# Kernel optimization log

Measured on AMD Instinct MI355X. Metric: run time of the kernel, lower is better.

The kernel has to match this reference:

```python
import jax, jax.numpy as jnp
import numpy as np

H = 10          # hidden_dim
OUT = 100       # linear output (charset logits)
STEPS = 30      # decoder steps
START = 1.0     # Alphabet.start_integer
NL = 3          # num_layers
B, L, TD, AD = 8192, 32, 63, 1
IN = TD + AD


def setup_inputs() -> dict:
    key = jax.random.key(0)
    ks = iter(jax.random.split(key, 64))
    s = 0.3
    d = {}
    d["families"] = jnp.zeros((B,), jnp.int32)
    d["languages"] = jnp.zeros((B,), jnp.int32)
    d["tags"] = jax.random.uniform(next(ks), (B, TD), jnp.float32)
    d["lemmata"] = jax.random.uniform(next(ks), (B, L), jnp.float32)
    for pre in ("enc", "dec"):
        for l in range(NL):
            din = IN if l == 0 else H
            d[f"{pre}_W_ih{l}"] = jax.random.normal(next(ks), (4 * H, din), jnp.float32) * s
            d[f"{pre}_W_hh{l}"] = jax.random.normal(next(ks), (4 * H, H), jnp.float32) * s
            d[f"{pre}_b_ih{l}"] = jax.random.normal(next(ks), (4 * H,), jnp.float32) * s
            d[f"{pre}_b_hh{l}"] = jax.random.normal(next(ks), (4 * H,), jnp.float32) * s
    d["lin_W"] = jax.random.normal(next(ks), (OUT, H), jnp.float32) * s
    d["lin_b"] = jnp.zeros((OUT,), jnp.float32)
    return d


def _lstm_cell(layers, h, c, x):
    # torch LSTM gate order: i, f, g, o. Dropout inactive in eval mode.
    nh, nc, inp = [], [], x
    for (W_ih, W_hh, b_ih, b_hh), hl, cl in zip(layers, h, c):
        g = inp @ W_ih.T + hl @ W_hh.T + b_ih + b_hh  # (B, 4H)
        i_, f_, g_, o_ = jnp.split(g, 4, axis=-1)
        cl = jax.nn.sigmoid(f_) * cl + jax.nn.sigmoid(i_) * jnp.tanh(g_)
        hl = jax.nn.sigmoid(o_) * jnp.tanh(cl)
        nh.append(hl); nc.append(cl); inp = hl
    return tuple(nh), tuple(nc), inp


def _forward(tags, lemmata, enc, dec, lin_W, lin_b):
    Bb, Ll = lemmata.shape
    # time-major encoder input: feature order [char, tags...] -> (L, B, 1+TD)
    xs = jnp.concatenate([lemmata.T[:, :, None],
                          jnp.broadcast_to(tags[None], (Ll, Bb, tags.shape[1]))], axis=-1)
    h = tuple(jnp.zeros((Bb, H), lemmata.dtype) for _ in range(NL))
    c = h

    def estep(carry, x):
        hh, cc = carry
        hh, cc, _ = _lstm_cell(enc, hh, cc, x)
        return (hh, cc), None

    (h, c), _ = jax.lax.scan(estep, (h, c), xs)

    tok = jnp.full((Bb,), START, lemmata.dtype)

    def dstep(carry, _):
        hh, cc, t = carry
        x = jnp.concatenate([t[:, None], tags], axis=-1)  # (B, 1+TD)
        hh, cc, y = _lstm_cell(dec, hh, cc, x)
        probs = jax.nn.sigmoid(y @ lin_W.T + lin_b)       # (B, 100)
        nt = jax.lax.stop_gradient(jnp.argmax(probs, axis=-1))
        return (hh, cc, nt.astype(t.dtype)), (probs, nt)

    _, (probs, toks) = jax.lax.scan(dstep, (h, c, tok), None, length=STEPS)
    return jnp.transpose(probs, (1, 0, 2)), toks.T  # (B,30,100), (B,30)


def reference(families, languages, tags, lemmata,
              enc_W_ih0, enc_W_hh0, enc_b_ih0, enc_b_hh0,
              enc_W_ih1, enc_W_hh1, enc_b_ih1, enc_b_hh1,
              enc_W_ih2, enc_W_hh2, enc_b_ih2, enc_b_hh2,
              dec_W_ih0, dec_W_hh0, dec_b_ih0, dec_b_hh0,
              dec_W_ih1, dec_W_hh1, dec_b_ih1, dec_b_hh1,
              dec_W_ih2, dec_W_hh2, dec_b_ih2, dec_b_hh2,
              lin_W, lin_b):
    enc = ((enc_W_ih0, enc_W_hh0, enc_b_ih0, enc_b_hh0),
           (enc_W_ih1, enc_W_hh1, enc_b_ih1, enc_b_hh1),
           (enc_W_ih2, enc_W_hh2, enc_b_ih2, enc_b_hh2))
    dec = ((dec_W_ih0, dec_W_hh0, dec_b_ih0, dec_b_hh0),
           (dec_W_ih1, dec_W_hh1, dec_b_ih1, dec_b_hh1),
           (dec_W_ih2, dec_W_hh2, dec_b_ih2, dec_b_hh2))
    return _forward(tags, lemmata, enc, dec, lin_W, lin_b)
```

## Files before the change

### kernel.cpp

```cpp
#include <hip/hip_runtime.h>
#include <cmath>

#define DEV __device__ __forceinline__

static DEV float fast_exp2(float x) {
#if __has_builtin(__builtin_amdgcn_exp2f)
  return __builtin_amdgcn_exp2f(x);
#else
  return exp2f(x);
#endif
}
static DEV float fast_rcp(float x) {
#if __has_builtin(__builtin_amdgcn_rcpf)
  return __builtin_amdgcn_rcpf(x);
#else
  return 1.0f / x;
#endif
}

#define LOG2E 1.4426950408889634f

static DEV float rdl(float x, int l) {
  return __int_as_float(__builtin_amdgcn_readlane(__float_as_int(x), l));
}

template <int K>
static DEV float qb(float x) {
  return __int_as_float(
      __builtin_amdgcn_update_dpp(0, __float_as_int(x), K * 0x55, 0xF, 0xF, true));
}

struct KP {
  const float* tags; const float* lem;
  const float* eWih0; const float* eWhh0; const float* ebih0; const float* ebhh0;
  const float* eWih1; const float* eWhh1; const float* ebih1; const float* ebhh1;
  const float* eWih2; const float* eWhh2; const float* ebih2; const float* ebhh2;
  const float* dWih0; const float* dWhh0; const float* dbih0; const float* dbhh0;
  const float* dWih1; const float* dWhh1; const float* dbih1; const float* dbhh1;
  const float* dWih2; const float* dWhh2; const float* dbih2; const float* dbhh2;
  const float* linW; const float* linb;
  float* outp; float* outt;
  int B;
};

__global__ __launch_bounds__(256) void seq2seq_kernel(KP P) {
  const int tid = threadIdx.x;
  const int lane = tid & 63;
  const int b = blockIdx.x * 4 + (tid >> 6);

  __shared__ float sW[5040];
  for (int i = tid; i < 5040; i += 256) {
    int m = (i >= 2520) ? 1 : 0;
    int r2 = i - m * 2520;
    int rr = r2 / 63;
    int dd = r2 - rr * 63;
    sW[i] = (m ? P.dWih0 : P.eWih0)[rr * 64 + 1 + dd];
  }
  __syncthreads();
  if (b >= P.B) return;

  const int jq = lane >> 2;
  const int kg = lane & 3;
  const int jj = (jq < 10) ? jq : 9;
  const int row = kg * 10 + jj;

  const float kc = (kg == 2) ? (-2.0f * LOG2E) : (-LOG2E);
  const float am = (kg == 2) ? 2.0f : 1.0f;
  const float ab = (kg == 2) ? -1.0f : 0.0f;

  auto act = [&](float g) -> float {
    float y = fast_rcp(1.0f + fast_exp2(g * kc));
    return fmaf(am, y, ab);
  };

  float tv = (lane < 63) ? P.tags[(size_t)b * 63 + lane] : 0.0f;
  float lemv = (lane < 32) ? P.lem[(size_t)b * 32 + lane] : 0.0f;

  float ew0c = P.eWih0[row * 64];
  float ehh0[10], eih1[10], ehh1[10], eih2[10], ehh2[10];
#pragma unroll
  for (int q = 0; q < 10; q++) {
    ehh0[q] = P.eWhh0[row * 10 + q];
    eih1[q] = P.eWih1[row * 10 + q];
    ehh1[q] = P.eWhh1[row * 10 + q];
    eih2[q] = P.eWih2[row * 10 + q];
    ehh2[q] = P.eWhh2[row * 10 + q];
  }
  float pre0 = P.ebih0[row] + P.ebhh0[row];
  float pre1 = P.ebih1[row] + P.ebhh1[row];
  float pre2 = P.ebih2[row] + P.ebhh2[row];
  float dpre0 = P.dbih0[row] + P.dbhh0[row];

  {
    const int ro = row * 63;
#pragma unroll
    for (int d = 0; d < 63; d++) {
      float ts = rdl(tv, d);
      pre0 = fmaf(sW[ro + d], ts, pre0);
      dpre0 = fmaf(sW[2520 + ro + d], ts, dpre0);
    }
  }

  float h0[10], h1[10], h2[10];
#pragma unroll
  for (int q = 0; q < 10; q++) { h0[q] = 0.0f; h1[q] = 0.0f; h2[q] = 0.0f; }
  float c0 = 0.0f, c1 = 0.0f, c2 = 0.0f;

  auto update = [&](float a, float& c, float (&h)[10]) {
    float a0 = qb<0>(a);
    float a1 = qb<1>(a);
    float a2 = qb<2>(a);
    float a3 = qb<3>(a);
    c = a1 * c + a0 * a2;
    float y = fast_rcp(1.0f + fast_exp2(c * (-2.0f * LOG2E)));
    float hv = a3 * fmaf(2.0f, y, -1.0f);
#pragma unroll
    for (int q = 0; q < 10; q++) h[q] = rdl(hv, 4 * q);
  };

  for (int t = 0; t < 32; t++) {
    float ch = rdl(lemv, t);
    float g = fmaf(ew0c, ch, pre0);
#pragma unroll
    for (int q = 0; q < 10; q++) g = fmaf(ehh0[q], h0[q], g);
    update(act(g), c0, h0);

    g = pre1;
#pragma unroll
    for (int q = 0; q < 10; q++) g = fmaf(eih1[q], h0[q], g);
#pragma unroll
    for (int q = 0; q < 10; q++) g = fmaf(ehh1[q], h1[q], g);
    update(act(g), c1, h1);

    g = pre2;
#pragma unroll
    for (int q = 0; q < 10; q++) g = fmaf(eih2[q], h1[q], g);
#pragma unroll
    for (int q = 0; q < 10; q++) g = fmaf(ehh2[q], h2[q], g);
    update(act(g), c2, h2);
  }

  float dw0c = P.dWih0[row * 64];
  float dhh0[10], dih1[10], dhh1[10], dih2[10], dhh2[10];
#pragma unroll
  for (int q = 0; q < 10; q++) {
    dhh0[q] = P.dWhh0[row * 10 + q];
    dih1[q] = P.dWih1[row * 10 + q];
    dhh1[q] = P.dWhh1[row * 10 + q];
    dih2[q] = P.dWih2[row * 10 + q];
    dhh2[q] = P.dWhh2[row * 10 + q];
  }
  float dpre1 = P.dbih1[row] + P.dbhh1[row];
  float dpre2 = P.dbih2[row] + P.dbhh2[row];

  const int lr1 = lane;
  const int lr2 = (lane < 36) ? (64 + lane) : 99;
  float lw0[10], lw1[10];
#pragma unroll
  for (int q = 0; q < 10; q++) {
    lw0[q] = P.linW[lr1 * 10 + q];
    lw1[q] = P.linW[lr2 * 10 + q];
  }
  float lb0 = P.linb[lr1];
  float lb1 = (lane < 36) ? P.linb[lr2] : -1e30f;

  float* op0 = P.outp + (size_t)b * 3000;
  float tok = 1.0f;
  float tokv = 0.0f;

  for (int s = 0; s < 30; s++) {
    float g = fmaf(dw0c, tok, dpre0);
#pragma unroll
    for (int q = 0; q < 10; q++) g = fmaf(dhh0[q], h0[q], g);
    update(act(g), c0, h0);

    g = dpre1;
#pragma unroll
    for (int q = 0; q < 10; q++) g = fmaf(dih1[q], h0[q], g);
#pragma unroll
    for (int q = 0; q < 10; q++) g = fmaf(dhh1[q], h1[q], g);
    update(act(g), c1, h1);

    g = dpre2;
#pragma unroll
    for (int q = 0; q < 10; q++) g = fmaf(dih2[q], h1[q], g);
#pragma unroll
    for (int q = 0; q < 10; q++) g = fmaf(dhh2[q], h2[q], g);
    update(act(g), c2, h2);

    float z0 = lb0, z1 = lb1;
#pragma unroll
    for (int q = 0; q < 10; q++) {
      z0 = fmaf(lw0[q], h2[q], z0);
      z1 = fmaf(lw1[q], h2[q], z1);
    }
    float p0 = fast_rcp(1.0f + fast_exp2(z0 * (-LOG2E)));
    float p1 = fast_rcp(1.0f + fast_exp2(z1 * (-LOG2E)));

    float* op = op0 + s * 100;
    op[lane] = p0;
    if (lane < 36) op[64 + lane] = p1;

    float vm = p0; int im = lane;
    if (p1 > vm) { vm = p1; im = 64 + lane; }
#pragma unroll
    for (int off = 32; off > 0; off >>= 1) {
      float vo = __shfl_xor(vm, off);
      int io = __shfl_xor(im, off);
      if (vo > vm || (vo == vm && io < im)) { vm = vo; im = io; }
    }
    im = __builtin_amdgcn_readfirstlane(im);
    tok = (float)im;
    tokv = (lane == s) ? tok : tokv;
  }

  if (lane < 30) P.outt[(size_t)b * 30 + lane] = tokv;
}

extern "C" void kernel_launch(void* const* d_in, const int* in_sizes, int n_in,
                              void* d_out, int out_size, void* d_ws, size_t ws_size,
                              hipStream_t stream) {
  KP P;
  P.tags = (const float*)d_in[2];
  P.lem = (const float*)d_in[3];
  P.eWih0 = (const float*)d_in[4];  P.eWhh0 = (const float*)d_in[5];
  P.ebih0 = (const float*)d_in[6];  P.ebhh0 = (const float*)d_in[7];
  P.eWih1 = (const float*)d_in[8];  P.eWhh1 = (const float*)d_in[9];
  P.ebih1 = (const float*)d_in[10]; P.ebhh1 = (const float*)d_in[11];
  P.eWih2 = (const float*)d_in[12]; P.eWhh2 = (const float*)d_in[13];
  P.ebih2 = (const float*)d_in[14]; P.ebhh2 = (const float*)d_in[15];
  P.dWih0 = (const float*)d_in[16]; P.dWhh0 = (const float*)d_in[17];
  P.dbih0 = (const float*)d_in[18]; P.dbhh0 = (const float*)d_in[19];
  P.dWih1 = (const float*)d_in[20]; P.dWhh1 = (const float*)d_in[21];
  P.dbih1 = (const float*)d_in[22]; P.dbhh1 = (const float*)d_in[23];
  P.dWih2 = (const float*)d_in[24]; P.dWhh2 = (const float*)d_in[25];
  P.dbih2 = (const float*)d_in[26]; P.dbhh2 = (const float*)d_in[27];
  P.linW = (const float*)d_in[28];
  P.linb = (const float*)d_in[29];

  const int B = in_sizes[3] / 32;
  P.B = B;
  P.outp = (float*)d_out;
  P.outt = P.outp + (size_t)B * 3000;

  const int blocks = (B + 3) / 4;
  seq2seq_kernel<<<dim3(blocks), dim3(256), 0, stream>>>(P);
}
```

Before: 180.9 us.

## Drop LDS weight staging, split dot-product chains, and use DPP argmax

The shared-memory staging of the layer-0 tag weights and its block barrier are removed. The tag projection is now computed from float4 global loads with readlane broadcasts. Each gate dot product uses two accumulators to shorten the FMA dependency chain. The shuffle-based argmax becomes a DPP row-shift max reduction followed by ballots and a count-trailing-zeros to pick the first maximal index. The DPP max and ballot path should cut the latency of each decoder step, but global loads in place of LDS could add some memory latency, and the tie handling now relies on exact float equality.

```diff
diff --git a/kernel.cpp b/kernel.cpp
--- a/kernel.cpp
+++ b/kernel.cpp
@@ -28,6 +28,23 @@
 static DEV float qb(float x) {
   return __int_as_float(
       __builtin_amdgcn_update_dpp(0, __float_as_int(x), K * 0x55, 0xF, 0xF, true));
+}
+
+template <int CTRL>
+static DEV float dppmax(float x) {
+  float o = __int_as_float(
+      __builtin_amdgcn_update_dpp(0, __float_as_int(x), CTRL, 0xF, 0xF, true));
+  return fmaxf(x, o);
+}
+
+static DEV float wavemax_bcast(float m) {
+  m = dppmax<0x111>(m);
+  m = dppmax<0x112>(m);
+  m = dppmax<0x114>(m);
+  m = dppmax<0x118>(m);
+  m = dppmax<0x142>(m);
+  m = dppmax<0x143>(m);
+  return rdl(m, 63);
 }
 
 struct KP {
@@ -47,16 +64,6 @@
   const int tid = threadIdx.x;
   const int lane = tid & 63;
   const int b = blockIdx.x * 4 + (tid >> 6);
-
-  __shared__ float sW[5040];
-  for (int i = tid; i < 5040; i += 256) {
-    int m = (i >= 2520) ? 1 : 0;
-    int r2 = i - m * 2520;
-    int rr = r2 / 63;
-    int dd = r2 - rr * 63;
-    sW[i] = (m ? P.dWih0 : P.eWih0)[rr * 64 + 1 + dd];
-  }
-  __syncthreads();
   if (b >= P.B) return;
 
   const int jq = lane >> 2;
@@ -76,7 +83,29 @@
   float tv = (lane < 63) ? P.tags[(size_t)b * 63 + lane] : 0.0f;
   float lemv = (lane < 32) ? P.lem[(size_t)b * 32 + lane] : 0.0f;
 
-  float ew0c = P.eWih0[row * 64];
+  float pre0 = P.ebih0[row] + P.ebhh0[row];
+  float dpre0 = P.dbih0[row] + P.dbhh0[row];
+  float ew0c, dw0c;
+  {
+    const float4* e4 = (const float4*)P.eWih0 + row * 16;
+    const float4* d4 = (const float4*)P.dWih0 + row * 16;
+    float4 we = e4[0], wd = d4[0];
+    ew0c = we.x; dw0c = wd.x;
+    float t0 = rdl(tv, 0), t1 = rdl(tv, 1), t2 = rdl(tv, 2);
+    pre0 = fmaf(we.y, t0, pre0); pre0 = fmaf(we.z, t1, pre0); pre0 = fmaf(we.w, t2, pre0);
+    dpre0 = fmaf(wd.y, t0, dpre0); dpre0 = fmaf(wd.z, t1, dpre0); dpre0 = fmaf(wd.w, t2, dpre0);
+#pragma unroll
+    for (int c = 1; c < 16; c++) {
+      float4 e = e4[c], d = d4[c];
+      int dd = 4 * c - 1;
+      float u0 = rdl(tv, dd), u1 = rdl(tv, dd + 1), u2 = rdl(tv, dd + 2), u3 = rdl(tv, dd + 3);
+      pre0 = fmaf(e.x, u0, pre0); pre0 = fmaf(e.y, u1, pre0);
+      pre0 = fmaf(e.z, u2, pre0); pre0 = fmaf(e.w, u3, pre0);
+      dpre0 = fmaf(d.x, u0, dpre0); dpre0 = fmaf(d.y, u1, dpre0);
+      dpre0 = fmaf(d.z, u2, dpre0); dpre0 = fmaf(d.w, u3, dpre0);
+    }
+  }
+
   float ehh0[10], eih1[10], ehh1[10], eih2[10], ehh2[10];
 #pragma unroll
   for (int q = 0; q < 10; q++) {
@@ -86,20 +115,8 @@
     eih2[q] = P.eWih2[row * 10 + q];
     ehh2[q] = P.eWhh2[row * 10 + q];
   }
-  float pre0 = P.ebih0[row] + P.ebhh0[row];
   float pre1 = P.ebih1[row] + P.ebhh1[row];
   float pre2 = P.ebih2[row] + P.ebhh2[row];
-  float dpre0 = P.dbih0[row] + P.dbhh0[row];
-
-  {
-    const int ro = row * 63;
-#pragma unroll
-    for (int d = 0; d < 63; d++) {
-      float ts = rdl(tv, d);
-      pre0 = fmaf(sW[ro + d], ts, pre0);
-      dpre0 = fmaf(sW[2520 + ro + d], ts, dpre0);
-    }
-  }
 
   float h0[10], h1[10], h2[10];
 #pragma unroll
@@ -111,36 +128,48 @@
     float a1 = qb<1>(a);
     float a2 = qb<2>(a);
     float a3 = qb<3>(a);
-    c = a1 * c + a0 * a2;
+    c = fmaf(a1, c, a0 * a2);
     float y = fast_rcp(1.0f + fast_exp2(c * (-2.0f * LOG2E)));
     float hv = a3 * fmaf(2.0f, y, -1.0f);
 #pragma unroll
     for (int q = 0; q < 10; q++) h[q] = rdl(hv, 4 * q);
   };
 
+  auto dot2 = [&](const float (&wa)[10], const float (&ha)[10],
+                  const float (&wb)[10], const float (&hb)[10], float pre) -> float {
+    float ga = pre, gb = 0.0f;
+#pragma unroll
+    for (int q = 0; q < 10; q += 2) {
+      ga = fmaf(wa[q], ha[q], ga);
+      gb = fmaf(wa[q + 1], ha[q + 1], gb);
+    }
+#pragma unroll
+    for (int q = 0; q < 10; q += 2) {
+      ga = fmaf(wb[q], hb[q], ga);
+      gb = fmaf(wb[q + 1], hb[q + 1], gb);
+    }
+    return ga + gb;
+  };
+  auto dot1 = [&](const float (&w)[10], const float (&h)[10], float pre) -> float {
+    float ga = pre, gb = 0.0f;
+#pragma unroll
+    for (int q = 0; q < 10; q += 2) {
+      ga = fmaf(w[q], h[q], ga);
+      gb = fmaf(w[q + 1], h[q + 1], gb);
+    }
+    return ga + gb;
+  };
+
   for (int t = 0; t < 32; t++) {
     float ch = rdl(lemv, t);
-    float g = fmaf(ew0c, ch, pre0);
-#pragma unroll
-    for (int q = 0; q < 10; q++) g = fmaf(ehh0[q], h0[q], g);
+    float g = dot1(ehh0, h0, fmaf(ew0c, ch, pre0));
     update(act(g), c0, h0);
-
-    g = pre1;
-#pragma unroll
-    for (int q = 0; q < 10; q++) g = fmaf(eih1[q], h0[q], g);
-#pragma unroll
-    for (int q = 0; q < 10; q++) g = fmaf(ehh1[q], h1[q], g);
+    g = dot2(eih1, h0, ehh1, h1, pre1);
     update(act(g), c1, h1);
-
-    g = pre2;
-#pragma unroll
-    for (int q = 0; q < 10; q++) g = fmaf(eih2[q], h1[q], g);
-#pragma unroll
-    for (int q = 0; q < 10; q++) g = fmaf(ehh2[q], h2[q], g);
+    g = dot2(eih2, h1, ehh2, h2, pre2);
     update(act(g), c2, h2);
   }
 
-  float dw0c = P.dWih0[row * 64];
   float dhh0[10], dih1[10], dhh1[10], dih2[10], dhh2[10];
 #pragma unroll
   for (int q = 0; q < 10; q++) {
@@ -153,15 +182,14 @@
   float dpre1 = P.dbih1[row] + P.dbhh1[row];
   float dpre2 = P.dbih2[row] + P.dbhh2[row];
 
-  const int lr1 = lane;
   const int lr2 = (lane < 36) ? (64 + lane) : 99;
   float lw0[10], lw1[10];
 #pragma unroll
   for (int q = 0; q < 10; q++) {
-    lw0[q] = P.linW[lr1 * 10 + q];
+    lw0[q] = P.linW[lane * 10 + q];
     lw1[q] = P.linW[lr2 * 10 + q];
   }
-  float lb0 = P.linb[lr1];
+  float lb0 = P.linb[lane];
   float lb1 = (lane < 36) ? P.linb[lr2] : -1e30f;
 
   float* op0 = P.outp + (size_t)b * 3000;
@@ -169,31 +197,15 @@
   float tokv = 0.0f;
 
   for (int s = 0; s < 30; s++) {
-    float g = fmaf(dw0c, tok, dpre0);
-#pragma unroll
-    for (int q = 0; q < 10; q++) g = fmaf(dhh0[q], h0[q], g);
+    float g = dot1(dhh0, h0, fmaf(dw0c, tok, dpre0));
     update(act(g), c0, h0);
-
-    g = dpre1;
-#pragma unroll
-    for (int q = 0; q < 10; q++) g = fmaf(dih1[q], h0[q], g);
-#pragma unroll
-    for (int q = 0; q < 10; q++) g = fmaf(dhh1[q], h1[q], g);
+    g = dot2(dih1, h0, dhh1, h1, dpre1);
     update(act(g), c1, h1);
-
-    g = dpre2;
-#pragma unroll
-    for (int q = 0; q < 10; q++) g = fmaf(dih2[q], h1[q], g);
-#pragma unroll
-    for (int q = 0; q < 10; q++) g = fmaf(dhh2[q], h2[q], g);
+    g = dot2(dih2, h1, dhh2, h2, dpre2);
     update(act(g), c2, h2);
 
-    float z0 = lb0, z1 = lb1;
-#pragma unroll
-    for (int q = 0; q < 10; q++) {
-      z0 = fmaf(lw0[q], h2[q], z0);
-      z1 = fmaf(lw1[q], h2[q], z1);
-    }
+    float z0 = dot1(lw0, h2, lb0);
+    float z1 = dot1(lw1, h2, lb1);
     float p0 = fast_rcp(1.0f + fast_exp2(z0 * (-LOG2E)));
     float p1 = fast_rcp(1.0f + fast_exp2(z1 * (-LOG2E)));
 
@@ -201,15 +213,10 @@
     op[lane] = p0;
     if (lane < 36) op[64 + lane] = p1;
 
-    float vm = p0; int im = lane;
-    if (p1 > vm) { vm = p1; im = 64 + lane; }
-#pragma unroll
-    for (int off = 32; off > 0; off >>= 1) {
-      float vo = __shfl_xor(vm, off);
-      int io = __shfl_xor(im, off);
-      if (vo > vm || (vo == vm && io < im)) { vm = vo; im = io; }
-    }
-    im = __builtin_amdgcn_readfirstlane(im);
+    float vm = wavemax_bcast(fmaxf(p0, p1));
+    unsigned long long m0 = __ballot(p0 == vm);
+    unsigned long long m1 = __ballot(p1 == vm);
+    int im = m0 ? (int)__builtin_ctzll(m0) : 64 + (int)__builtin_ctzll(m1);
     tok = (float)im;
     tokv = (lane == s) ? tok : tokv;
   }
```

Result: faster. 175.0 us (-3.2%).
